# Optimization experiments

Measured on AMD Instinct MI355X. Metric: run time of the kernel, lower is better.

## Reference

```python
import jax, jax.numpy as jnp
import numpy as np

MARGIN = 1.0
EPS = 1e-6  # torch F.pairwise_distance default eps, added elementwise to (x - y)
NEG_INF = -1e30
POS_INF = 1e30


def _pairwise_dist_matrix(e):
    # D[i,j] = || e_i - e_j + EPS ||_2, expanded so we never materialize [B,B,D]:
    # ||d + eps||^2 = ||d||^2 + 2*eps*sum(d) + Dfeat*eps^2,  d = e_i - e_j
    sq = jnp.sum(e * e, axis=1)          # [B]
    s = jnp.sum(e, axis=1)               # [B]
    d2 = (sq[:, None] + sq[None, :] - 2.0 * (e @ e.T)
          + 2.0 * EPS * (s[:, None] - s[None, :])
          + e.shape[1] * (EPS * EPS))
    return jnp.sqrt(jnp.maximum(d2, 0.0))  # [B,B]


def _pdist(x, y):
    # F.pairwise_distance(p=2): ||x - y + eps||
    return jnp.sqrt(jnp.sum(jnp.square(x - y + EPS), axis=-1))


def setup_inputs() -> dict:
    B, D = 4096, 128
    key = jax.random.key(0)
    k1, k2, k3, k4 = jax.random.split(key, 4)
    embedding = jax.random.normal(k1, (B, D), dtype=jnp.float32)
    # label space == batch, each label appears exactly once in the batch
    target_idx = jax.random.permutation(k2, B).astype(jnp.int32)
    positive_idxs = jax.random.bernoulli(k3, 0.02, (B, B))  # [B, L] label-space mask
    negative_idxs = jax.random.bernoulli(k4, 0.5, (B, B))
    return {"embedding": embedding, "target_idx": target_idx,
            "positive_idxs": positive_idxs, "negative_idxs": negative_idxs}


def reference(embedding, target_idx, positive_idxs, negative_idxs):
    # Mining happens under no_grad in the original module.
    dm = jax.lax.stop_gradient(_pairwise_dist_matrix(embedding))  # [B,B]
    # batch j is a positive/negative candidate for anchor i iff its label is flagged
    pos_mask = positive_idxs[:, target_idx]  # [B,B] bool
    neg_mask = negative_idxs[:, target_idx]
    pos_idx = jnp.argmax(jnp.where(pos_mask, dm, NEG_INF), axis=1)  # hardest positive
    neg_idx = jnp.argmin(jnp.where(neg_mask, dm, POS_INF), axis=1)  # hardest negative
    valid = jnp.any(pos_mask, axis=1) & jnp.any(neg_mask, axis=1)
    a = embedding
    p = embedding[pos_idx]
    n = embedding[neg_idx]
    ap = _pdist(a, p)
    an = _pdist(a, n)
    pn = _pdist(p, n)
    loss = jax.nn.relu(ap - jnp.minimum(an, pn) + MARGIN)
    w = valid.astype(loss.dtype)
    return jnp.sum(loss * w) / jnp.maximum(jnp.sum(w), 1.0)
```

## Files before the change

kernel.cpp:

```cpp
#include <hip/hip_runtime.h>
#include <stdint.h>

#define BN 4096
#define DD 128
#define EPSF 1e-6f
#define MARGINF 1.0f

typedef unsigned long long ull;
typedef unsigned short ushort;
typedef short short8 __attribute__((ext_vector_type(8)));
typedef float f32x4 __attribute__((ext_vector_type(4)));

__device__ __forceinline__ unsigned int ord_f32(float f) {
    unsigned int u = __float_as_uint(f);
    return (u & 0x80000000u) ? ~u : (u | 0x80000000u);
}
__device__ __forceinline__ ushort bf16_rne(float x) {
    unsigned int u = __float_as_uint(x);
    return (ushort)((u + 0x7FFFu + ((u >> 16) & 1u)) >> 16);
}

__global__ __launch_bounds__(256)
void k_prep(const float* __restrict__ e, const int* __restrict__ tidx,
            const int* __restrict__ pos, const int* __restrict__ neg,
            float* __restrict__ rjp, unsigned int* __restrict__ jn,
            ull* __restrict__ pkey, ull* __restrict__ nkey,
            unsigned int* __restrict__ ehi, unsigned int* __restrict__ eperm,
            ull* __restrict__ pbits, ull* __restrict__ nbits) {
    const int w = threadIdx.x >> 6, lane = threadIdx.x & 63;
    const int row = blockIdx.x * 4 + w;
    const int c = tidx[row];
    float2 v = ((const float2*)(e + (size_t)row * DD))[lane];
    ushort hx = bf16_rne(v.x), hy = bf16_rne(v.y);
    unsigned int packed = (unsigned int)hx | ((unsigned int)hy << 16);
    ehi[row * 64 + lane] = packed;
    eperm[(size_t)c * 64 + lane] = packed;
    float ss = v.x + v.y;
    float qq = v.x * v.x + v.y * v.y;
    #pragma unroll
    for (int off = 32; off > 0; off >>= 1) {
        ss += __shfl_down(ss, off);
        qq += __shfl_down(qq, off);
    }
    if (lane == 0) {
        rjp[c] = qq - 2.0f * EPSF * ss;
        jn[c] = 0xFFFFFFFFu - (unsigned int)row;
        pkey[row] = 0ULL; nkey[row] = 0ULL;
    }

    const int* prow = pos + (size_t)row * BN;
    const int* nrow = neg + (size_t)row * BN;
    ull myp = 0ULL, myn = 0ULL;
    #pragma unroll
    for (int j0 = 0; j0 < 64; j0 += 16) {
        int pv[16], nv[16];
        #pragma unroll
        for (int k = 0; k < 16; k++)
            pv[k] = __builtin_nontemporal_load(prow + (j0 + k) * 64 + lane);
        #pragma unroll
        for (int k = 0; k < 16; k++)
            nv[k] = __builtin_nontemporal_load(nrow + (j0 + k) * 64 + lane);
        #pragma unroll
        for (int k = 0; k < 16; k++) {
            ull bp = __ballot(pv[k] != 0);
            ull bn = __ballot(nv[k] != 0);
            if (lane == j0 + k) { myp = bp; myn = bn; }
        }
    }
    pbits[(size_t)row * 64 + lane] = myp;
    nbits[(size_t)row * 64 + lane] = myn;
}

__global__ __launch_bounds__(256, 4)
void k_select(const ushort* __restrict__ ehi, const ushort* __restrict__ eperm,
              const ull* __restrict__ pbits, const ull* __restrict__ nbits,
              const float* __restrict__ rjp, const unsigned int* __restrict__ jn,
              ull* __restrict__ pkey, ull* __restrict__ nkey) {
    __shared__ float rjL[1024];
    __shared__ unsigned int jnL[1024];
    __shared__ ull bitP[256], bitN[256];
    __shared__ ull scrp[64], scrn[64];

    const int tid = threadIdx.x;
    const int lane = tid & 63, w = tid >> 6;
    const int lrow = lane & 15, quad = lane >> 4;
    const int r0 = blockIdx.x * 16;
    const int c0 = blockIdx.y * 1024;
    const int cb0 = c0 >> 6;
    const int shft = w * 16 + lrow;

    #pragma unroll
    for (int k = 0; k < 4; k++) {
        int idx = k * 256 + tid;
        rjL[idx] = rjp[c0 + idx];
        jnL[idx] = jn[c0 + idx];
    }
    bitP[tid] = pbits[(size_t)(r0 + (tid >> 4)) * 64 + cb0 + (tid & 15)];
    bitN[tid] = nbits[(size_t)(r0 + (tid >> 4)) * 64 + cb0 + (tid & 15)];

    short8 a[4];
    #pragma unroll
    for (int ks = 0; ks < 4; ks++)
        a[ks] = *(const short8*)(ehi + (size_t)(r0 + lrow) * DD + ks * 32 + quad * 8);

    __syncthreads();

    ull kp[4] = {0ULL, 0ULL, 0ULL, 0ULL};
    ull kn[4] = {0ULL, 0ULL, 0ULL, 0ULL};

    short8 bf[2][4];
    float rjc[2]; unsigned int jni[2];

#define LOADTILE(BUF, JT) do {                                                  \
        const int lcol = (JT) * 64 + shft;                                      \
        rjc[BUF] = rjL[lcol];                                                   \
        jni[BUF] = jnL[lcol];                                                   \
        const ushort* bp = eperm + (size_t)(c0 + lcol) * DD + quad * 8;         \
        _Pragma("unroll")                                                       \
        for (int ks = 0; ks < 4; ks++)                                          \
            bf[BUF][ks] = *(const short8*)(bp + ks * 32);                       \
    } while (0)

    LOADTILE(0, 0);

    #pragma unroll
    for (int jt = 0; jt < 16; jt++) {
        const int cur = jt & 1, nxt = cur ^ 1;
        if (jt < 15) {
            if (nxt == 0) LOADTILE(0, jt + 1); else LOADTILE(1, jt + 1);
        }
        f32x4 acc = (f32x4){0.f, 0.f, 0.f, 0.f};
        #pragma unroll
        for (int ks = 0; ks < 4; ks++)
            acc = __builtin_amdgcn_mfma_f32_16x16x32_bf16(a[ks], bf[cur][ks], acc, 0, 0, 0);
        #pragma unroll
        for (int t = 0; t < 4; t++) {
            ull pw = bitP[(quad * 4 + t) * 16 + jt];
            ull nw = bitN[(quad * 4 + t) * 16 + jt];
            float m = rjc[cur] - 2.0f * acc[t];
            unsigned int om = ord_f32(m);
            ull keyp = ((ull)om << 32) | (ull)jni[cur];
            ull keyn = ((ull)(om ^ 0xFFFFFFFFu) << 32) | (ull)jni[cur];
            if (((pw >> shft) & 1ULL) && keyp > kp[t]) kp[t] = keyp;
            if (((nw >> shft) & 1ULL) && keyn > kn[t]) kn[t] = keyn;
        }
    }
#undef LOADTILE

    #pragma unroll
    for (int t = 0; t < 4; t++) {
        #pragma unroll
        for (int off = 8; off > 0; off >>= 1) {
            ull o = __shfl_xor(kp[t], off); if (o > kp[t]) kp[t] = o;
            o = __shfl_xor(kn[t], off);     if (o > kn[t]) kn[t] = o;
        }
        if (lrow == 0) {
            scrp[(quad * 4 + t) * 4 + w] = kp[t];
            scrn[(quad * 4 + t) * 4 + w] = kn[t];
        }
    }
    __syncthreads();
    if (tid < 16) {
        ull xp = 0ULL, xn = 0ULL;
        #pragma unroll
        for (int k = 0; k < 4; k++) {
            ull v = scrp[tid * 4 + k]; if (v > xp) xp = v;
            v = scrn[tid * 4 + k];     if (v > xn) xn = v;
        }
        if (xp) atomicMax(&pkey[r0 + tid], xp);
        if (xn) atomicMax(&nkey[r0 + tid], xn);
    }
}

__global__ void k_loss(const float* __restrict__ e,
                       const ull* __restrict__ pkey, const ull* __restrict__ nkey,
                       float* __restrict__ partials) {
    int w = threadIdx.x >> 6, lane = threadIdx.x & 63;
    int row = blockIdx.x * 4 + w;
    ull pk = pkey[row], nk = nkey[row];
    float loss = 0.0f, wt = 0.0f;
    if (pk != 0ULL && nk != 0ULL) {
        int pi = (int)(0xFFFFFFFFu - (unsigned)(pk & 0xFFFFFFFFu));
        int ni = (int)(0xFFFFFFFFu - (unsigned)(nk & 0xFFFFFFFFu));
        float2 av = ((const float2*)(e + (size_t)row * DD))[lane];
        float2 pv = ((const float2*)(e + (size_t)pi * DD))[lane];
        float2 nv = ((const float2*)(e + (size_t)ni * DD))[lane];
        float dx, dy;
        dx = av.x - pv.x + EPSF; dy = av.y - pv.y + EPSF;
        float ap2 = dx * dx + dy * dy;
        dx = av.x - nv.x + EPSF; dy = av.y - nv.y + EPSF;
        float an2 = dx * dx + dy * dy;
        dx = pv.x - nv.x + EPSF; dy = pv.y - nv.y + EPSF;
        float pn2 = dx * dx + dy * dy;
        #pragma unroll
        for (int off = 32; off > 0; off >>= 1) {
            ap2 += __shfl_down(ap2, off);
            an2 += __shfl_down(an2, off);
            pn2 += __shfl_down(pn2, off);
        }
        if (lane == 0) {
            float ap = sqrtf(ap2), an = sqrtf(an2), pn = sqrtf(pn2);
            loss = fmaxf(ap - fminf(an, pn) + MARGINF, 0.0f);
            wt = 1.0f;
        }
    }
    __shared__ float sl[4], sw[4];
    if (lane == 0) { sl[w] = loss; sw[w] = wt; }
    __syncthreads();
    if (threadIdx.x == 0) {
        partials[blockIdx.x * 2 + 0] = sl[0] + sl[1] + sl[2] + sl[3];
        partials[blockIdx.x * 2 + 1] = sw[0] + sw[1] + sw[2] + sw[3];
    }
}

__global__ void k_final(const float* __restrict__ partials, float* __restrict__ out) {
    int tid = threadIdx.x;
    float L = 0.0f, W = 0.0f;
    for (int i = 0; i < 4; i++) {
        int idx = tid + i * 256;
        L += partials[idx * 2];
        W += partials[idx * 2 + 1];
    }
    #pragma unroll
    for (int off = 32; off > 0; off >>= 1) {
        L += __shfl_down(L, off);
        W += __shfl_down(W, off);
    }
    __shared__ float sl[4], sw[4];
    int w = tid >> 6, lane = tid & 63;
    if (lane == 0) { sl[w] = L; sw[w] = W; }
    __syncthreads();
    if (tid == 0) {
        float Lt = sl[0] + sl[1] + sl[2] + sl[3];
        float Wt = sw[0] + sw[1] + sw[2] + sw[3];
        out[0] = Lt / fmaxf(Wt, 1.0f);
    }
}

extern "C" void kernel_launch(void* const* d_in, const int* in_sizes, int n_in,
                              void* d_out, int out_size, void* d_ws, size_t ws_size,
                              hipStream_t stream) {
    const float* e    = (const float*)d_in[0];
    const int*   tidx = (const int*)d_in[1];
    const int*   pos  = (const int*)d_in[2];
    const int*   neg  = (const int*)d_in[3];
    float* out = (float*)d_out;

    char* p = (char*)d_ws;
    ull* pkey  = (ull*)p;                 p += (size_t)BN * 8;
    ull* nkey  = (ull*)p;                 p += (size_t)BN * 8;
    float* rjp = (float*)p;               p += (size_t)BN * 4;
    unsigned int* jn = (unsigned int*)p;  p += (size_t)BN * 4;
    float* partials = (float*)p;          p += 2048 * 4;
    unsigned int* ehi = (unsigned int*)p;   p += (size_t)BN * 64 * 4;
    unsigned int* eperm = (unsigned int*)p; p += (size_t)BN * 64 * 4;
    ull* pbits = (ull*)p;                 p += (size_t)BN * 64 * 8;
    ull* nbits = (ull*)p;                 p += (size_t)BN * 64 * 8;

    k_prep<<<BN / 4, 256, 0, stream>>>(e, tidx, pos, neg, rjp, jn,
                                       pkey, nkey, ehi, eperm, pbits, nbits);
    dim3 grid(BN / 16, 4);
    k_select<<<grid, 256, 0, stream>>>((const ushort*)ehi, (const ushort*)eperm,
                                       pbits, nbits, rjp, jn, pkey, nkey);
    k_loss<<<BN / 4, 256, 0, stream>>>(e, pkey, nkey, partials);
    k_final<<<1, 256, 0, stream>>>(partials, out);
}
```

Measured before the change: 186.5 us.

## Fuse hardest-sample selection and loss into one kernel, dropping column split and atomics

```diff
diff --git a/kernel.cpp b/kernel.cpp
--- a/kernel.cpp
+++ b/kernel.cpp
@@ -24,7 +24,6 @@
 void k_prep(const float* __restrict__ e, const int* __restrict__ tidx,
             const int* __restrict__ pos, const int* __restrict__ neg,
             float* __restrict__ rjp, unsigned int* __restrict__ jn,
-            ull* __restrict__ pkey, ull* __restrict__ nkey,
             unsigned int* __restrict__ ehi, unsigned int* __restrict__ eperm,
             ull* __restrict__ pbits, ull* __restrict__ nbits) {
     const int w = threadIdx.x >> 6, lane = threadIdx.x & 63;
@@ -45,7 +44,6 @@
     if (lane == 0) {
         rjp[c] = qq - 2.0f * EPSF * ss;
         jn[c] = 0xFFFFFFFFu - (unsigned int)row;
-        pkey[row] = 0ULL; nkey[row] = 0ULL;
     }
 
     const int* prow = pos + (size_t)row * BN;
@@ -71,32 +69,38 @@
     nbits[(size_t)row * 64 + lane] = myn;
 }
 
-__global__ __launch_bounds__(256, 4)
-void k_select(const ushort* __restrict__ ehi, const ushort* __restrict__ eperm,
-              const ull* __restrict__ pbits, const ull* __restrict__ nbits,
-              const float* __restrict__ rjp, const unsigned int* __restrict__ jn,
-              ull* __restrict__ pkey, ull* __restrict__ nkey) {
-    __shared__ float rjL[1024];
-    __shared__ unsigned int jnL[1024];
-    __shared__ ull bitP[256], bitN[256];
-    __shared__ ull scrp[64], scrn[64];
+__global__ __launch_bounds__(512, 4)
+void k_sel_loss(const float* __restrict__ e,
+                const ushort* __restrict__ ehi, const ushort* __restrict__ eperm,
+                const ull* __restrict__ pbits, const ull* __restrict__ nbits,
+                const float* __restrict__ rjp, const unsigned int* __restrict__ jn,
+                float* __restrict__ partials) {
+    __shared__ float rjL[4096];
+    __shared__ unsigned int jnL[4096];
+    __shared__ ull bitP[16 * 65], bitN[16 * 65];
+    __shared__ ull scrp[16 * 8], scrn[16 * 8];
+    __shared__ ull fkp[16], fkn[16];
+    __shared__ float lossL[16], wtL[16];
 
     const int tid = threadIdx.x;
     const int lane = tid & 63, w = tid >> 6;
     const int lrow = lane & 15, quad = lane >> 4;
     const int r0 = blockIdx.x * 16;
-    const int c0 = blockIdx.y * 1024;
-    const int cb0 = c0 >> 6;
-    const int shft = w * 16 + lrow;
-
-    #pragma unroll
-    for (int k = 0; k < 4; k++) {
-        int idx = k * 256 + tid;
-        rjL[idx] = rjp[c0 + idx];
-        jnL[idx] = jn[c0 + idx];
-    }
-    bitP[tid] = pbits[(size_t)(r0 + (tid >> 4)) * 64 + cb0 + (tid & 15)];
-    bitN[tid] = nbits[(size_t)(r0 + (tid >> 4)) * 64 + cb0 + (tid & 15)];
+    const int wof = w >> 2;
+    const int shft = (w & 3) * 16 + lrow;
+
+    #pragma unroll
+    for (int k = 0; k < 8; k++) {
+        int idx = k * 512 + tid;
+        rjL[idx] = rjp[idx];
+        jnL[idx] = jn[idx];
+    }
+    #pragma unroll
+    for (int k = 0; k < 2; k++) {
+        int idx = k * 512 + tid;
+        bitP[(idx >> 6) * 65 + (idx & 63)] = pbits[(size_t)(r0 + (idx >> 6)) * 64 + (idx & 63)];
+        bitN[(idx >> 6) * 65 + (idx & 63)] = nbits[(size_t)(r0 + (idx >> 6)) * 64 + (idx & 63)];
+    }
 
     short8 a[4];
     #pragma unroll
@@ -112,40 +116,43 @@
     float rjc[2]; unsigned int jni[2];
 
 #define LOADTILE(BUF, JT) do {                                                  \
-        const int lcol = (JT) * 64 + shft;                                      \
+        const int lcol = (JT) * 128 + w * 16 + lrow;                            \
         rjc[BUF] = rjL[lcol];                                                   \
         jni[BUF] = jnL[lcol];                                                   \
-        const ushort* bp = eperm + (size_t)(c0 + lcol) * DD + quad * 8;         \
+        const ushort* bp = eperm + (size_t)lcol * DD + quad * 8;                \
         _Pragma("unroll")                                                       \
         for (int ks = 0; ks < 4; ks++)                                          \
             bf[BUF][ks] = *(const short8*)(bp + ks * 32);                       \
     } while (0)
 
+#define COMPUTE(BUF, JT) do {                                                   \
+        f32x4 acc = (f32x4){0.f, 0.f, 0.f, 0.f};                                \
+        _Pragma("unroll")                                                       \
+        for (int ks = 0; ks < 4; ks++)                                          \
+            acc = __builtin_amdgcn_mfma_f32_16x16x32_bf16(a[ks], bf[BUF][ks], acc, 0, 0, 0); \
+        _Pragma("unroll")                                                       \
+        for (int t = 0; t < 4; t++) {                                           \
+            ull pw = bitP[(quad * 4 + t) * 65 + 2 * (JT) + wof];                \
+            ull nw = bitN[(quad * 4 + t) * 65 + 2 * (JT) + wof];                \
+            float m = rjc[BUF] - 2.0f * acc[t];                                 \
+            unsigned int om = ord_f32(m);                                       \
+            ull keyp = ((ull)om << 32) | (ull)jni[BUF];                         \
+            ull keyn = ((ull)(om ^ 0xFFFFFFFFu) << 32) | (ull)jni[BUF];         \
+            if (((pw >> shft) & 1ULL) && keyp > kp[t]) kp[t] = keyp;            \
+            if (((nw >> shft) & 1ULL) && keyn > kn[t]) kn[t] = keyn;            \
+        }                                                                       \
+    } while (0)
+
     LOADTILE(0, 0);
-
-    #pragma unroll
-    for (int jt = 0; jt < 16; jt++) {
-        const int cur = jt & 1, nxt = cur ^ 1;
-        if (jt < 15) {
-            if (nxt == 0) LOADTILE(0, jt + 1); else LOADTILE(1, jt + 1);
-        }
-        f32x4 acc = (f32x4){0.f, 0.f, 0.f, 0.f};
-        #pragma unroll
-        for (int ks = 0; ks < 4; ks++)
-            acc = __builtin_amdgcn_mfma_f32_16x16x32_bf16(a[ks], bf[cur][ks], acc, 0, 0, 0);
-        #pragma unroll
-        for (int t = 0; t < 4; t++) {
-            ull pw = bitP[(quad * 4 + t) * 16 + jt];
-            ull nw = bitN[(quad * 4 + t) * 16 + jt];
-            float m = rjc[cur] - 2.0f * acc[t];
-            unsigned int om = ord_f32(m);
-            ull keyp = ((ull)om << 32) | (ull)jni[cur];
-            ull keyn = ((ull)(om ^ 0xFFFFFFFFu) << 32) | (ull)jni[cur];
-            if (((pw >> shft) & 1ULL) && keyp > kp[t]) kp[t] = keyp;
-            if (((nw >> shft) & 1ULL) && keyn > kn[t]) kn[t] = keyn;
-        }
+    for (int jt2 = 0; jt2 < 16; jt2++) {
+        const int jA = 2 * jt2, jB = 2 * jt2 + 1;
+        LOADTILE(1, jB);
+        COMPUTE(0, jA);
+        if (jt2 < 15) LOADTILE(0, jB + 1);
+        COMPUTE(1, jB);
     }
 #undef LOADTILE
+#undef COMPUTE
 
     #pragma unroll
     for (int t = 0; t < 4; t++) {
@@ -155,72 +162,68 @@
             o = __shfl_xor(kn[t], off);     if (o > kn[t]) kn[t] = o;
         }
         if (lrow == 0) {
-            scrp[(quad * 4 + t) * 4 + w] = kp[t];
-            scrn[(quad * 4 + t) * 4 + w] = kn[t];
+            scrp[(quad * 4 + t) * 8 + w] = kp[t];
+            scrn[(quad * 4 + t) * 8 + w] = kn[t];
         }
     }
     __syncthreads();
     if (tid < 16) {
         ull xp = 0ULL, xn = 0ULL;
         #pragma unroll
-        for (int k = 0; k < 4; k++) {
-            ull v = scrp[tid * 4 + k]; if (v > xp) xp = v;
-            v = scrn[tid * 4 + k];     if (v > xn) xn = v;
-        }
-        if (xp) atomicMax(&pkey[r0 + tid], xp);
-        if (xn) atomicMax(&nkey[r0 + tid], xn);
-    }
-}
-
-__global__ void k_loss(const float* __restrict__ e,
-                       const ull* __restrict__ pkey, const ull* __restrict__ nkey,
-                       float* __restrict__ partials) {
-    int w = threadIdx.x >> 6, lane = threadIdx.x & 63;
-    int row = blockIdx.x * 4 + w;
-    ull pk = pkey[row], nk = nkey[row];
-    float loss = 0.0f, wt = 0.0f;
-    if (pk != 0ULL && nk != 0ULL) {
-        int pi = (int)(0xFFFFFFFFu - (unsigned)(pk & 0xFFFFFFFFu));
-        int ni = (int)(0xFFFFFFFFu - (unsigned)(nk & 0xFFFFFFFFu));
-        float2 av = ((const float2*)(e + (size_t)row * DD))[lane];
-        float2 pv = ((const float2*)(e + (size_t)pi * DD))[lane];
-        float2 nv = ((const float2*)(e + (size_t)ni * DD))[lane];
-        float dx, dy;
-        dx = av.x - pv.x + EPSF; dy = av.y - pv.y + EPSF;
-        float ap2 = dx * dx + dy * dy;
-        dx = av.x - nv.x + EPSF; dy = av.y - nv.y + EPSF;
-        float an2 = dx * dx + dy * dy;
-        dx = pv.x - nv.x + EPSF; dy = pv.y - nv.y + EPSF;
-        float pn2 = dx * dx + dy * dy;
-        #pragma unroll
-        for (int off = 32; off > 0; off >>= 1) {
-            ap2 += __shfl_down(ap2, off);
-            an2 += __shfl_down(an2, off);
-            pn2 += __shfl_down(pn2, off);
-        }
-        if (lane == 0) {
-            float ap = sqrtf(ap2), an = sqrtf(an2), pn = sqrtf(pn2);
-            loss = fmaxf(ap - fminf(an, pn) + MARGINF, 0.0f);
-            wt = 1.0f;
-        }
-    }
-    __shared__ float sl[4], sw[4];
-    if (lane == 0) { sl[w] = loss; sw[w] = wt; }
-    __syncthreads();
-    if (threadIdx.x == 0) {
-        partials[blockIdx.x * 2 + 0] = sl[0] + sl[1] + sl[2] + sl[3];
-        partials[blockIdx.x * 2 + 1] = sw[0] + sw[1] + sw[2] + sw[3];
+        for (int k = 0; k < 8; k++) {
+            ull v = scrp[tid * 8 + k]; if (v > xp) xp = v;
+            v = scrn[tid * 8 + k];     if (v > xn) xn = v;
+        }
+        fkp[tid] = xp; fkn[tid] = xn;
+    }
+    __syncthreads();
+
+    #pragma unroll
+    for (int rr = 0; rr < 2; rr++) {
+        const int r16 = w * 2 + rr;
+        const int row = r0 + r16;
+        ull pk = fkp[r16], nk = fkn[r16];
+        float loss = 0.0f, wt = 0.0f;
+        if (pk != 0ULL && nk != 0ULL) {
+            int pi = (int)(0xFFFFFFFFu - (unsigned)(pk & 0xFFFFFFFFu));
+            int ni = (int)(0xFFFFFFFFu - (unsigned)(nk & 0xFFFFFFFFu));
+            float2 av = ((const float2*)(e + (size_t)row * DD))[lane];
+            float2 pv = ((const float2*)(e + (size_t)pi * DD))[lane];
+            float2 nv = ((const float2*)(e + (size_t)ni * DD))[lane];
+            float dx, dy;
+            dx = av.x - pv.x + EPSF; dy = av.y - pv.y + EPSF;
+            float ap2 = dx * dx + dy * dy;
+            dx = av.x - nv.x + EPSF; dy = av.y - nv.y + EPSF;
+            float an2 = dx * dx + dy * dy;
+            dx = pv.x - nv.x + EPSF; dy = pv.y - nv.y + EPSF;
+            float pn2 = dx * dx + dy * dy;
+            #pragma unroll
+            for (int off = 32; off > 0; off >>= 1) {
+                ap2 += __shfl_down(ap2, off);
+                an2 += __shfl_down(an2, off);
+                pn2 += __shfl_down(pn2, off);
+            }
+            if (lane == 0) {
+                float ap = sqrtf(ap2), an = sqrtf(an2), pn = sqrtf(pn2);
+                loss = fmaxf(ap - fminf(an, pn) + MARGINF, 0.0f);
+                wt = 1.0f;
+            }
+        }
+        if (lane == 0) { lossL[r16] = loss; wtL[r16] = wt; }
+    }
+    __syncthreads();
+    if (tid == 0) {
+        float L = 0.0f, W = 0.0f;
+        #pragma unroll
+        for (int k = 0; k < 16; k++) { L += lossL[k]; W += wtL[k]; }
+        partials[blockIdx.x * 2 + 0] = L;
+        partials[blockIdx.x * 2 + 1] = W;
     }
 }
 
 __global__ void k_final(const float* __restrict__ partials, float* __restrict__ out) {
     int tid = threadIdx.x;
-    float L = 0.0f, W = 0.0f;
-    for (int i = 0; i < 4; i++) {
-        int idx = tid + i * 256;
-        L += partials[idx * 2];
-        W += partials[idx * 2 + 1];
-    }
+    float L = partials[tid * 2], W = partials[tid * 2 + 1];
     #pragma unroll
     for (int off = 32; off > 0; off >>= 1) {
         L += __shfl_down(L, off);
@@ -247,21 +250,17 @@
     float* out = (float*)d_out;
 
     char* p = (char*)d_ws;
-    ull* pkey  = (ull*)p;                 p += (size_t)BN * 8;
-    ull* nkey  = (ull*)p;                 p += (size_t)BN * 8;
     float* rjp = (float*)p;               p += (size_t)BN * 4;
     unsigned int* jn = (unsigned int*)p;  p += (size_t)BN * 4;
-    float* partials = (float*)p;          p += 2048 * 4;
+    float* partials = (float*)p;          p += 512 * 4;
     unsigned int* ehi = (unsigned int*)p;   p += (size_t)BN * 64 * 4;
     unsigned int* eperm = (unsigned int*)p; p += (size_t)BN * 64 * 4;
     ull* pbits = (ull*)p;                 p += (size_t)BN * 64 * 8;
     ull* nbits = (ull*)p;                 p += (size_t)BN * 64 * 8;
 
     k_prep<<<BN / 4, 256, 0, stream>>>(e, tidx, pos, neg, rjp, jn,
-                                       pkey, nkey, ehi, eperm, pbits, nbits);
-    dim3 grid(BN / 16, 4);
-    k_select<<<grid, 256, 0, stream>>>((const ushort*)ehi, (const ushort*)eperm,
-                                       pbits, nbits, rjp, jn, pkey, nkey);
-    k_loss<<<BN / 4, 256, 0, stream>>>(e, pkey, nkey, partials);
+                                       ehi, eperm, pbits, nbits);
+    k_sel_loss<<<BN / 16, 512, 0, stream>>>(e, (const ushort*)ehi, (const ushort*)eperm,
+                                            pbits, nbits, rjp, jn, partials);
     k_final<<<1, 256, 0, stream>>>(partials, out);
 }
```

New measurement: 182.1 us. 1.02x faster.
